# Optimization experiments

Hardware: AMD Instinct MI355X
Metric: run time of the kernel (lower is better)

## Reference

```python
import jax, jax.numpy as jnp
import numpy as np

N, DEG, IN_DIM, HID, OUT = 50000, 32, 256, 256, 128

def setup_inputs() -> dict:
    key = jax.random.key(0)
    k1, k2, k3, k4, k5, k6 = jax.random.split(key, 6)
    node_features = jax.random.normal(k1, (N, IN_DIM), dtype=jnp.float32)
    neighbor_idx = jax.random.randint(k2, (N, DEG), 0, N)
    scale1 = 1.0 / np.sqrt(2 * IN_DIM)
    scale2 = 1.0 / np.sqrt(HID)
    W1 = jax.random.normal(k3, (HID, 2 * IN_DIM), dtype=jnp.float32) * scale1
    b1 = jax.random.normal(k4, (HID,), dtype=jnp.float32) * scale1
    W2 = jax.random.normal(k5, (OUT, HID), dtype=jnp.float32) * scale2
    b2 = jax.random.normal(k6, (OUT,), dtype=jnp.float32) * scale2
    return {"node_features": node_features, "neighbor_idx": neighbor_idx,
            "W1": W1, "b1": b1, "W2": W2, "b2": b2}

def reference(node_features, neighbor_idx, W1, b1, W2, b2):
    # Layer 0 (mean aggregator, with neighbors):
    # gather [N, DEG, IN_DIM] neighbor features, mean over DEG
    nbr_mean = jnp.mean(node_features[neighbor_idx], axis=1)  # [N, IN_DIM]
    combined = jnp.concatenate([node_features, nbr_mean], axis=-1)  # [N, 2*IN_DIM]
    h = jax.nn.relu(combined @ W1.T + b1)  # [N, HID]
    # Layer 1: empty neighbor list -> linear_without_neighbors + relu
    out = jax.nn.relu(h @ W2.T + b2)  # [N, OUT]
    return out
```

## Files before the change

### kernel.cpp

```cpp
#include <hip/hip_runtime.h>
#include <stdint.h>

#define N_NODES 50000
#define DEG     32
#define IN_DIM  256
#define K1      512
#define HID     256
#define OUT_DIM 128

#define NCHUNK  4
#define CDIM    64
#define SLICE8  ((size_t)N_NODES * CDIM)
#define GT      16

#define MT     64
#define NTILES 782
#define GBLK   256
#define CSTR   520
#define HSTR   264

typedef __bf16 bf16x8 __attribute__((ext_vector_type(8)));
typedef float  f32x4  __attribute__((ext_vector_type(4)));
typedef float  f32x2  __attribute__((ext_vector_type(2)));

__device__ __forceinline__ unsigned short f2bf(float f) {
    union { float f; unsigned u; } v; v.f = f;
    unsigned r = v.u + 0x7fffu + ((v.u >> 16) & 1u);
    return (unsigned short)(r >> 16);
}
__device__ __forceinline__ int clampN(int v) {
    return v < 0 ? 0 : (v >= N_NODES ? N_NODES - 1 : v);
}

#define FEAT_BLKS ((N_NODES + 7) / 8)
__global__ __launch_bounds__(256)
void prep_all(const float* __restrict__ feat,
              const float* __restrict__ W1, const float* __restrict__ W2,
              const int*   __restrict__ nbr,
              unsigned short* __restrict__ featb,
              unsigned char*  __restrict__ featF8,
              unsigned short* __restrict__ W1b, unsigned short* __restrict__ W2b,
              unsigned short* __restrict__ nbr16)
{
    const int t = threadIdx.x;
    if (blockIdx.x < FEAT_BLKS) {
        const int node = blockIdx.x * 8 + (t >> 5);
        const int seg  = t & 31;
        if (node < N_NODES) {
            const float4* src = (const float4*)(feat + (size_t)node * IN_DIM + seg * 8);
            float4 f0 = src[0], f1 = src[1];
            ushort4 o0, o1;
            o0.x = f2bf(f0.x); o0.y = f2bf(f0.y); o0.z = f2bf(f0.z); o0.w = f2bf(f0.w);
            o1.x = f2bf(f1.x); o1.y = f2bf(f1.y); o1.z = f2bf(f1.z); o1.w = f2bf(f1.w);
            unsigned short* db = featb + (size_t)node * IN_DIM + seg * 8;
            *(ushort4*)db       = o0;
            *(ushort4*)(db + 4) = o1;
            int u0 = 0, u1 = 0;
            u0 = __builtin_amdgcn_cvt_pk_fp8_f32(f0.x, f0.y, u0, false);
            u0 = __builtin_amdgcn_cvt_pk_fp8_f32(f0.z, f0.w, u0, true);
            u1 = __builtin_amdgcn_cvt_pk_fp8_f32(f1.x, f1.y, u1, false);
            u1 = __builtin_amdgcn_cvt_pk_fp8_f32(f1.z, f1.w, u1, true);
            const int c   = seg >> 3;
            const int off = (seg & 7) * 8;
            unsigned char* d8 = featF8 + (size_t)c * SLICE8 + (size_t)node * CDIM + off;
            ((int*)d8)[0] = u0;
            ((int*)d8)[1] = u1;
        }
    } else {
        const int bid = blockIdx.x - FEAT_BLKS;
        const int stride = 256 * 256 * 4;
        const int tid4 = (bid * 256 + t) * 4;
        for (int i = tid4; i < HID * K1; i += stride) {
            float4 f = *(const float4*)(W1 + i);
            ushort4 o; o.x = f2bf(f.x); o.y = f2bf(f.y); o.z = f2bf(f.z); o.w = f2bf(f.w);
            *(ushort4*)(W1b + i) = o;
        }
        for (int i = tid4; i < OUT_DIM * HID; i += stride) {
            float4 f = *(const float4*)(W2 + i);
            ushort4 o; o.x = f2bf(f.x); o.y = f2bf(f.y); o.z = f2bf(f.z); o.w = f2bf(f.w);
            *(ushort4*)(W2b + i) = o;
        }
        for (int i = tid4; i < N_NODES * DEG; i += stride) {
            int4 v = *(const int4*)(nbr + i);
            ushort4 o;
            o.x = (unsigned short)clampN(v.x); o.y = (unsigned short)clampN(v.y);
            o.z = (unsigned short)clampN(v.z); o.w = (unsigned short)clampN(v.w);
            *(ushort4*)(nbr16 + i) = o;
        }
    }
}

__global__ __launch_bounds__(256)
void gather_mean_fp8(const unsigned char*  __restrict__ featF8,
                     const unsigned short* __restrict__ nbr16,
                     unsigned short*       __restrict__ meanb)
{
    __shared__ unsigned short sIdx[GT * DEG];
    const int tid  = threadIdx.x;
    const int c    = blockIdx.y;
    const int base = blockIdx.x * GT;

    if (tid < 128) {
        *(ushort4*)(sIdx + tid * 4) =
            *(const ushort4*)(nbr16 + (size_t)base * DEG + tid * 4);
    }
    __syncthreads();

    const unsigned char* slice = featF8 + (size_t)c * SLICE8;
    const int grp = tid >> 4;
    const int ln  = tid & 15;
    const unsigned short* idxr = sIdx + grp * DEG;

    float s0 = 0.f, s1 = 0.f, s2 = 0.f, s3 = 0.f;
    #pragma unroll 8
    for (int j = 0; j < DEG; ++j) {
        int nb = idxr[j];
        unsigned v = *(const unsigned*)(slice + (size_t)nb * CDIM + ln * 4);
        f32x2 lo = __builtin_amdgcn_cvt_pk_f32_fp8(v, false);
        f32x2 hi = __builtin_amdgcn_cvt_pk_f32_fp8(v, true);
        s0 += lo[0]; s1 += lo[1]; s2 += hi[0]; s3 += hi[1];
    }
    const float sc = 1.0f / 32.0f;
    ushort4 o;
    o.x = f2bf(s0 * sc); o.y = f2bf(s1 * sc);
    o.z = f2bf(s2 * sc); o.w = f2bf(s3 * sc);
    const int node = base + grp;
    *(ushort4*)(meanb + (size_t)node * IN_DIM + c * CDIM + ln * 4) = o;
}

__global__ __launch_bounds__(512, 2)
void sage_gemm_reg(const unsigned short* __restrict__ featb,
                   const unsigned short* __restrict__ meanb,
                   const unsigned short* __restrict__ W1b,
                   const float*          __restrict__ b1,
                   const unsigned short* __restrict__ W2b,
                   const float*          __restrict__ b2,
                   float*                __restrict__ out)
{
    __shared__ __align__(16) unsigned short sC[MT * CSTR];
    __shared__ __align__(16) unsigned short sH[MT * HSTR];

    const int tid  = threadIdx.x;
    const int lane = tid & 63;
    const int wave = tid >> 6;
    const int r    = lane & 15;
    const int q    = lane >> 4;

    bf16x8 w1f[2][16];
    #pragma unroll
    for (int nt = 0; nt < 2; ++nt) {
        const size_t nrow = (size_t)(wave * 32 + nt * 16 + r) * K1;
        #pragma unroll
        for (int kk = 0; kk < 16; ++kk)
            w1f[nt][kk] = *(const bf16x8*)(W1b + nrow + kk * 32 + q * 8);
    }
    bf16x8 w2f[8];
    {
        const size_t orow = (size_t)(wave * 16 + r) * HID;
        #pragma unroll
        for (int kk = 0; kk < 8; ++kk)
            w2f[kk] = *(const bf16x8*)(W2b + orow + kk * 32 + q * 8);
    }
    const float bias1a = b1[wave * 32 + r];
    const float bias1b = b1[wave * 32 + 16 + r];
    const float bias2  = b2[wave * 16 + r];

    for (int tile = blockIdx.x; tile < NTILES; tile += GBLK) {
        const int base = tile * MT;

        for (int i = wave * 8; i < wave * 8 + 8; ++i) {
            const int node = base + i;
            if (node < N_NODES) {
                const unsigned short* src = (lane < 32)
                    ? featb + (size_t)node * IN_DIM + lane * 8
                    : meanb + (size_t)node * IN_DIM + (lane - 32) * 8;
                *(bf16x8*)(&sC[i * CSTR + lane * 8]) = *(const bf16x8*)src;
            } else {
                bf16x8 z = (bf16x8){0, 0, 0, 0, 0, 0, 0, 0};
                *(bf16x8*)(&sC[i * CSTR + lane * 8]) = z;
            }
        }
        __syncthreads();

        {
            f32x4 acc[4][2];
            #pragma unroll
            for (int mt = 0; mt < 4; ++mt)
                #pragma unroll
                for (int nt = 0; nt < 2; ++nt)
                    acc[mt][nt] = (f32x4){0.f, 0.f, 0.f, 0.f};

            #pragma unroll
            for (int kk = 0; kk < 16; ++kk) {
                bf16x8 a[4];
                #pragma unroll
                for (int mt = 0; mt < 4; ++mt)
                    a[mt] = *(const bf16x8*)(&sC[(mt * 16 + r) * CSTR + kk * 32 + q * 8]);
                #pragma unroll
                for (int nt = 0; nt < 2; ++nt)
                    #pragma unroll
                    for (int mt = 0; mt < 4; ++mt)
                        acc[mt][nt] = __builtin_amdgcn_mfma_f32_16x16x32_bf16(a[mt], w1f[nt][kk], acc[mt][nt], 0, 0, 0);
            }
            #pragma unroll
            for (int nt = 0; nt < 2; ++nt) {
                const int n = wave * 32 + nt * 16 + r;
                const float bias = nt ? bias1b : bias1a;
                #pragma unroll
                for (int mt = 0; mt < 4; ++mt)
                    #pragma unroll
                    for (int g = 0; g < 4; ++g) {
                        const int m = mt * 16 + q * 4 + g;
                        float v = acc[mt][nt][g] + bias;
                        sH[m * HSTR + n] = f2bf(v > 0.f ? v : 0.f);
                    }
            }
        }
        __syncthreads();

        {
            f32x4 acc3[4];
            #pragma unroll
            for (int mt = 0; mt < 4; ++mt) acc3[mt] = (f32x4){0.f, 0.f, 0.f, 0.f};

            #pragma unroll
            for (int kk = 0; kk < 8; ++kk)
                #pragma unroll
                for (int mt = 0; mt < 4; ++mt) {
                    bf16x8 a = *(const bf16x8*)(&sH[(mt * 16 + r) * HSTR + kk * 32 + q * 8]);
                    acc3[mt] = __builtin_amdgcn_mfma_f32_16x16x32_bf16(a, w2f[kk], acc3[mt], 0, 0, 0);
                }

            const int o = wave * 16 + r;
            #pragma unroll
            for (int mt = 0; mt < 4; ++mt)
                #pragma unroll
                for (int g = 0; g < 4; ++g) {
                    const int m = mt * 16 + q * 4 + g;
                    const int node = base + m;
                    if (node < N_NODES) {
                        float v = acc3[mt][g] + bias2;
                        out[(size_t)node * OUT_DIM + o] = v > 0.f ? v : 0.f;
                    }
                }
        }
    }
}

__global__ __launch_bounds__(256)
void sage_naive(const float* __restrict__ feat, const int* __restrict__ nbr,
                const float* __restrict__ W1, const float* __restrict__ b1,
                const float* __restrict__ W2, const float* __restrict__ b2,
                float* __restrict__ out) {
    __shared__ float comb[K1];
    __shared__ float h[HID];
    const int node = blockIdx.x;
    const int t = threadIdx.x;
    comb[t] = feat[(size_t)node * IN_DIM + t];
    float acc = 0.f;
    for (int d = 0; d < DEG; ++d) {
        int nb = clampN(nbr[node * DEG + d]);
        acc += feat[(size_t)nb * IN_DIM + t];
    }
    comb[IN_DIM + t] = acc * (1.0f / 32.0f);
    __syncthreads();
    float s = b1[t];
    for (int k = 0; k < K1; ++k) s += comb[k] * W1[(size_t)t * K1 + k];
    h[t] = s > 0.f ? s : 0.f;
    __syncthreads();
    if (t < OUT_DIM) {
        float s2 = b2[t];
        for (int k = 0; k < HID; ++k) s2 += h[k] * W2[(size_t)t * HID + k];
        out[(size_t)node * OUT_DIM + t] = s2 > 0.f ? s2 : 0.f;
    }
}

extern "C" void kernel_launch(void* const* d_in, const int* in_sizes, int n_in,
                              void* d_out, int out_size, void* d_ws, size_t ws_size,
                              hipStream_t stream) {
    const float* feat = (const float*)d_in[0];
    const int*   nbr  = (const int*)d_in[1];
    const float* W1   = (const float*)d_in[2];
    const float* b1   = (const float*)d_in[3];
    const float* W2   = (const float*)d_in[4];
    const float* b2   = (const float*)d_in[5];
    float* out = (float*)d_out;

    const size_t feat_elems = (size_t)N_NODES * IN_DIM;
    const size_t w1_elems   = (size_t)HID * K1;
    const size_t w2_elems   = (size_t)OUT_DIM * HID;
    const size_t mean_elems = (size_t)N_NODES * IN_DIM;
    const size_t idx_elems  = (size_t)N_NODES * DEG;
    const size_t u16_elems  = feat_elems + w1_elems + w2_elems + mean_elems + idx_elems;
    const size_t need = u16_elems * sizeof(unsigned short)
                      + (size_t)NCHUNK * SLICE8;

    if (ws_size >= need) {
        unsigned short* featb  = (unsigned short*)d_ws;
        unsigned short* W1b    = featb + feat_elems;
        unsigned short* W2b    = W1b + w1_elems;
        unsigned short* meanb  = W2b + w2_elems;
        unsigned short* nbr16  = meanb + mean_elems;
        unsigned char*  featF8 = (unsigned char*)(nbr16 + idx_elems);

        prep_all<<<FEAT_BLKS + 256, 256, 0, stream>>>(feat, W1, W2, nbr,
                                                      featb, featF8, W1b, W2b, nbr16);
        gather_mean_fp8<<<dim3(N_NODES / GT, NCHUNK), 256, 0, stream>>>(featF8, nbr16, meanb);
        sage_gemm_reg<<<GBLK, 512, 0, stream>>>(featb, meanb, W1b, b1, W2b, b2, out);
    } else {
        sage_naive<<<N_NODES, 256, 0, stream>>>(feat, nbr, W1, b1, W2, b2, out);
    }
}
```

Measured before the change: 187.1 us.

## Double-buffer GEMM tiles with async LDS loads and batch gather loads

The fused GEMM kernel now stages each tile of node features and neighbour means straight into LDS with global_load_lds. It double-buffers those tiles so the next tile's load overlaps the current tile's MFMA work, and halves the tile to 32 rows to make room for the second buffer. The gather kernel issues all 32 neighbour loads into registers before converting and summing, to raise memory-level parallelism. Weight fragments are pinned in registers with empty asm statements. The async copies rely on the barrier also waiting on outstanding LDS-DMA loads, and the smaller tile halves the reuse of the register-resident weights per tile.

Result: faster. 174.3 us (-6.9%).

```diff
diff --git a/kernel.cpp b/kernel.cpp
--- a/kernel.cpp
+++ b/kernel.cpp
@@ -13,8 +13,8 @@
 #define SLICE8  ((size_t)N_NODES * CDIM)
 #define GT      16
 
-#define MT     64
-#define NTILES 782
+#define MT     32
+#define NTILES ((N_NODES + MT - 1) / MT)
 #define GBLK   256
 #define CSTR   520
 #define HSTR   264
@@ -22,6 +22,8 @@
 typedef __bf16 bf16x8 __attribute__((ext_vector_type(8)));
 typedef float  f32x4  __attribute__((ext_vector_type(4)));
 typedef float  f32x2  __attribute__((ext_vector_type(2)));
+
+#define PIN(x) asm volatile("" : "+v"(x))
 
 __device__ __forceinline__ unsigned short f2bf(float f) {
     union { float f; unsigned u; } v; v.f = f;
@@ -30,6 +32,11 @@
 }
 __device__ __forceinline__ int clampN(int v) {
     return v < 0 ? 0 : (v >= N_NODES ? N_NODES - 1 : v);
+}
+__device__ __forceinline__ void async_copy16(const void* g, void* l) {
+    __builtin_amdgcn_global_load_lds(
+        (const __attribute__((address_space(1))) void*)g,
+        (__attribute__((address_space(3))) void*)l, 16, 0, 0);
 }
 
 #define FEAT_BLKS ((N_NODES + 7) / 8)
@@ -111,13 +118,17 @@
     const int ln  = tid & 15;
     const unsigned short* idxr = sIdx + grp * DEG;
 
-    float s0 = 0.f, s1 = 0.f, s2 = 0.f, s3 = 0.f;
-    #pragma unroll 8
+    unsigned vv[DEG];
+    #pragma unroll
     for (int j = 0; j < DEG; ++j) {
         int nb = idxr[j];
-        unsigned v = *(const unsigned*)(slice + (size_t)nb * CDIM + ln * 4);
-        f32x2 lo = __builtin_amdgcn_cvt_pk_f32_fp8(v, false);
-        f32x2 hi = __builtin_amdgcn_cvt_pk_f32_fp8(v, true);
+        vv[j] = *(const unsigned*)(slice + (size_t)nb * CDIM + ln * 4);
+    }
+    float s0 = 0.f, s1 = 0.f, s2 = 0.f, s3 = 0.f;
+    #pragma unroll
+    for (int j = 0; j < DEG; ++j) {
+        f32x2 lo = __builtin_amdgcn_cvt_pk_f32_fp8(vv[j], false);
+        f32x2 hi = __builtin_amdgcn_cvt_pk_f32_fp8(vv[j], true);
         s0 += lo[0]; s1 += lo[1]; s2 += hi[0]; s3 += hi[1];
     }
     const float sc = 1.0f / 32.0f;
@@ -129,15 +140,15 @@
 }
 
 __global__ __launch_bounds__(512, 2)
-void sage_gemm_reg(const unsigned short* __restrict__ featb,
-                   const unsigned short* __restrict__ meanb,
-                   const unsigned short* __restrict__ W1b,
-                   const float*          __restrict__ b1,
-                   const unsigned short* __restrict__ W2b,
-                   const float*          __restrict__ b2,
-                   float*                __restrict__ out)
+void sage_gemm_dbuf(const unsigned short* __restrict__ featb,
+                    const unsigned short* __restrict__ meanb,
+                    const unsigned short* __restrict__ W1b,
+                    const float*          __restrict__ b1,
+                    const unsigned short* __restrict__ W2b,
+                    const float*          __restrict__ b2,
+                    float*                __restrict__ out)
 {
-    __shared__ __align__(16) unsigned short sC[MT * CSTR];
+    __shared__ __align__(16) unsigned short sC[2][MT * CSTR];
     __shared__ __align__(16) unsigned short sH[MT * HSTR];
 
     const int tid  = threadIdx.x;
@@ -151,63 +162,71 @@
     for (int nt = 0; nt < 2; ++nt) {
         const size_t nrow = (size_t)(wave * 32 + nt * 16 + r) * K1;
         #pragma unroll
-        for (int kk = 0; kk < 16; ++kk)
+        for (int kk = 0; kk < 16; ++kk) {
             w1f[nt][kk] = *(const bf16x8*)(W1b + nrow + kk * 32 + q * 8);
+            PIN(w1f[nt][kk]);
+        }
     }
     bf16x8 w2f[8];
     {
         const size_t orow = (size_t)(wave * 16 + r) * HID;
         #pragma unroll
-        for (int kk = 0; kk < 8; ++kk)
+        for (int kk = 0; kk < 8; ++kk) {
             w2f[kk] = *(const bf16x8*)(W2b + orow + kk * 32 + q * 8);
+            PIN(w2f[kk]);
+        }
     }
     const float bias1a = b1[wave * 32 + r];
     const float bias1b = b1[wave * 32 + 16 + r];
     const float bias2  = b2[wave * 16 + r];
 
-    for (int tile = blockIdx.x; tile < NTILES; tile += GBLK) {
+    auto stage = [&](int tile, int buf) {
         const int base = tile * MT;
-
-        for (int i = wave * 8; i < wave * 8 + 8; ++i) {
-            const int node = base + i;
-            if (node < N_NODES) {
-                const unsigned short* src = (lane < 32)
-                    ? featb + (size_t)node * IN_DIM + lane * 8
-                    : meanb + (size_t)node * IN_DIM + (lane - 32) * 8;
-                *(bf16x8*)(&sC[i * CSTR + lane * 8]) = *(const bf16x8*)src;
-            } else {
-                bf16x8 z = (bf16x8){0, 0, 0, 0, 0, 0, 0, 0};
-                *(bf16x8*)(&sC[i * CSTR + lane * 8]) = z;
-            }
-        }
+        #pragma unroll
+        for (int j = 0; j < 4; ++j) {
+            const int i = wave * 4 + j;
+            int node = base + i;
+            if (node >= N_NODES) node = N_NODES - 1;
+            const unsigned short* g = (lane < 32)
+                ? featb + (size_t)node * IN_DIM + lane * 8
+                : meanb + (size_t)node * IN_DIM + (lane - 32) * 8;
+            async_copy16(g, &sC[buf][i * CSTR]);
+        }
+    };
+
+    int tile = blockIdx.x;
+    if (tile < NTILES) stage(tile, 0);
+    int buf = 0;
+
+    for (; tile < NTILES; tile += GBLK) {
         __syncthreads();
 
+        const int nxt = tile + GBLK;
+        if (nxt < NTILES) stage(nxt, buf ^ 1);
+
         {
-            f32x4 acc[4][2];
-            #pragma unroll
-            for (int mt = 0; mt < 4; ++mt)
+            f32x4 acc[2][2];
+            #pragma unroll
+            for (int mt = 0; mt < 2; ++mt)
                 #pragma unroll
                 for (int nt = 0; nt < 2; ++nt)
                     acc[mt][nt] = (f32x4){0.f, 0.f, 0.f, 0.f};
 
             #pragma unroll
             for (int kk = 0; kk < 16; ++kk) {
-                bf16x8 a[4];
-                #pragma unroll
-                for (int mt = 0; mt < 4; ++mt)
-                    a[mt] = *(const bf16x8*)(&sC[(mt * 16 + r) * CSTR + kk * 32 + q * 8]);
-                #pragma unroll
-                for (int nt = 0; nt < 2; ++nt)
-                    #pragma unroll
-                    for (int mt = 0; mt < 4; ++mt)
-                        acc[mt][nt] = __builtin_amdgcn_mfma_f32_16x16x32_bf16(a[mt], w1f[nt][kk], acc[mt][nt], 0, 0, 0);
+                bf16x8 a0 = *(const bf16x8*)(&sC[buf][r * CSTR + kk * 32 + q * 8]);
+                bf16x8 a1 = *(const bf16x8*)(&sC[buf][(16 + r) * CSTR + kk * 32 + q * 8]);
+                acc[0][0] = __builtin_amdgcn_mfma_f32_16x16x32_bf16(a0, w1f[0][kk], acc[0][0], 0, 0, 0);
+                acc[1][0] = __builtin_amdgcn_mfma_f32_16x16x32_bf16(a1, w1f[0][kk], acc[1][0], 0, 0, 0);
+                acc[0][1] = __builtin_amdgcn_mfma_f32_16x16x32_bf16(a0, w1f[1][kk], acc[0][1], 0, 0, 0);
+                acc[1][1] = __builtin_amdgcn_mfma_f32_16x16x32_bf16(a1, w1f[1][kk], acc[1][1], 0, 0, 0);
             }
             #pragma unroll
             for (int nt = 0; nt < 2; ++nt) {
                 const int n = wave * 32 + nt * 16 + r;
                 const float bias = nt ? bias1b : bias1a;
                 #pragma unroll
-                for (int mt = 0; mt < 4; ++mt)
+                for (int mt = 0; mt < 2; ++mt)
                     #pragma unroll
                     for (int g = 0; g < 4; ++g) {
                         const int m = mt * 16 + q * 4 + g;
@@ -219,21 +238,20 @@
         __syncthreads();
 
         {
-            f32x4 acc3[4];
-            #pragma unroll
-            for (int mt = 0; mt < 4; ++mt) acc3[mt] = (f32x4){0.f, 0.f, 0.f, 0.f};
-
-            #pragma unroll
-            for (int kk = 0; kk < 8; ++kk)
-                #pragma unroll
-                for (int mt = 0; mt < 4; ++mt) {
-                    bf16x8 a = *(const bf16x8*)(&sH[(mt * 16 + r) * HSTR + kk * 32 + q * 8]);
-                    acc3[mt] = __builtin_amdgcn_mfma_f32_16x16x32_bf16(a, w2f[kk], acc3[mt], 0, 0, 0);
-                }
-
+            f32x4 acc3[2];
+            acc3[0] = (f32x4){0.f, 0.f, 0.f, 0.f};
+            acc3[1] = (f32x4){0.f, 0.f, 0.f, 0.f};
+            #pragma unroll
+            for (int kk = 0; kk < 8; ++kk) {
+                bf16x8 h0 = *(const bf16x8*)(&sH[r * HSTR + kk * 32 + q * 8]);
+                bf16x8 h1 = *(const bf16x8*)(&sH[(16 + r) * HSTR + kk * 32 + q * 8]);
+                acc3[0] = __builtin_amdgcn_mfma_f32_16x16x32_bf16(h0, w2f[kk], acc3[0], 0, 0, 0);
+                acc3[1] = __builtin_amdgcn_mfma_f32_16x16x32_bf16(h1, w2f[kk], acc3[1], 0, 0, 0);
+            }
+            const int base = tile * MT;
             const int o = wave * 16 + r;
             #pragma unroll
-            for (int mt = 0; mt < 4; ++mt)
+            for (int mt = 0; mt < 2; ++mt)
                 #pragma unroll
                 for (int g = 0; g < 4; ++g) {
                     const int m = mt * 16 + q * 4 + g;
@@ -244,6 +262,7 @@
                     }
                 }
         }
+        buf ^= 1;
     }
 }
 
@@ -306,7 +325,7 @@
         prep_all<<<FEAT_BLKS + 256, 256, 0, stream>>>(feat, W1, W2, nbr,
                                                       featb, featF8, W1b, W2b, nbr16);
         gather_mean_fp8<<<dim3(N_NODES / GT, NCHUNK), 256, 0, stream>>>(featF8, nbr16, meanb);
-        sage_gemm_reg<<<GBLK, 512, 0, stream>>>(featb, meanb, W1b, b1, W2b, b2, out);
+        sage_gemm_dbuf<<<GBLK, 512, 0, stream>>>(featb, meanb, W1b, b1, W2b, b2, out);
     } else {
         sage_naive<<<N_NODES, 256, 0, stream>>>(feat, nbr, W1, b1, W2, b2, out);
     }
```
